# Performance work log

Measured on AMD Instinct MI355X. Metric: run time of the kernel, lower is better.

The kernel has to match this reference:

```python
import jax, jax.numpy as jnp
import numpy as np

# direction id -> (lat_shift, lon_shift)
WIND_DIRS = [(0, 0), (-1, 0), (-1, 1), (0, 1), (1, 1), (1, 0), (1, -1), (0, -1), (-1, -1)]
SWIN_SHIFT = (1, 3, 6)       # (pl, lat, lon)
WIND_SHIFT_SCALE = 2
LAT_REGIONS, LON_REGIONS = 4, 8
NUM_DIRS = 9


def setup_inputs() -> dict:
    key = jax.random.key(0)
    k1, k2 = jax.random.split(key)
    x = jax.random.normal(k1, (2, 14, 128, 256, 96), dtype=jnp.float32)
    wind_direction_id = jax.random.randint(k2, (2, 128, 256), 0, NUM_DIRS)
    return {"x": x, "wind_direction_id": wind_direction_id}


def _regional_dominant_dirs(wid):
    # wid: (B, H, W) int -> (B, LAT_REGIONS, LON_REGIONS) dominant direction per region
    B, H, W = wid.shape
    r = wid.reshape(B, LAT_REGIONS, H // LAT_REGIONS, LON_REGIONS, W // LON_REGIONS)
    counts = jnp.sum(jax.nn.one_hot(r, NUM_DIRS, dtype=jnp.float32), axis=(2, 4))  # (B, latR, lonR, 9)
    return jnp.argmax(counts, axis=-1)  # ties -> first max, matching torch bincount().argmax()


def reference(x, wind_direction_id):
    # x: (B, Pl, Lat, Lon, C); wind_direction_id: (B, H, W) in [0, 9)
    B, Pl, Lat, Lon, C = x.shape
    # 1) Swin fixed shift (negative roll on Pl, Lat, Lon)
    sp, sl, so = SWIN_SHIFT
    x = jnp.roll(x, (-sp, -sl, -so), axis=(1, 2, 3))
    # 2) per-region dominant wind direction
    rd = _regional_dominant_dirs(wind_direction_id)  # (B, latR, lonR)
    # nearest-neighbor upsample to full grid (matches F.interpolate mode='nearest')
    ih = (jnp.arange(Lat) * LAT_REGIONS) // Lat
    iw = (jnp.arange(Lon) * LON_REGIONS) // Lon
    dirs_up = rd[:, ih][:, :, iw]  # (B, Lat, Lon)
    # 3) mask & combine over the 9 rolled versions
    combined = jnp.zeros_like(x)
    for dir_id, (lat_s, lon_s) in enumerate(WIND_DIRS):
        als, alo = lat_s * WIND_SHIFT_SCALE, lon_s * WIND_SHIFT_SCALE
        shifted = x if (als == 0 and alo == 0) else jnp.roll(x, (als, alo), axis=(2, 3))
        mask = (dirs_up == dir_id).astype(x.dtype)[:, None, :, :, None]  # (B,1,Lat,Lon,1)
        combined = combined + shifted * mask
    # 4) global dominant direction (returned as stat)
    counts = jnp.bincount(wind_direction_id.reshape(-1), length=NUM_DIRS)
    dominant_id = jnp.argmax(counts)
    return combined, dominant_id
```

## Files before the change

kernel.cpp:

```cpp
#include <hip/hip_runtime.h>

namespace {
constexpr int kB   = 2;
constexpr int kPl  = 14;
constexpr int kLat = 128;
constexpr int kLon = 256;
constexpr int kC   = 96;
constexpr int kNumDirs = 9;
constexpr int kC4  = kC / 4;
constexpr int kNTotal = kB * kPl * kLat * kLon * kC;
constexpr int kRegions = kB * 4 * 8;
constexpr int kRowTasks = kB * kPl * kLat;
constexpr int kRowF4 = kLon * kC4;
constexpr int kRowIters = kRowF4 / 256;
}

typedef float f4 __attribute__((ext_vector_type(4)));

__device__ __constant__ int c_lat_s[kNumDirs] = {0,-1,-1, 0, 1, 1, 1, 0,-1};
__device__ __constant__ int c_lon_s[kNumDirs] = {0, 0, 1, 1, 1, 0,-1,-1,-1};

__global__ __launch_bounds__(256) void region_dirs_kernel(
        const int* __restrict__ wid, int* __restrict__ rdpack,
        int* __restrict__ cnt_blk) {
    __shared__ int cnt[kNumDirs];
    const int t = threadIdx.x;
    if (t < kNumDirs) cnt[t] = 0;
    __syncthreads();

    const int blk  = blockIdx.x;
    const int rlon = blk & 7;
    const int rlat = (blk >> 3) & 3;
    const int b    = blk >> 5;

    for (int k = t; k < 1024; k += 256) {
        const int i  = k >> 5;
        const int j  = k & 31;
        const int la = rlat * 32 + i;
        const int lo = rlon * 32 + j;
        atomicAdd(&cnt[wid[(b * kLat + la) * kLon + lo]], 1);
    }
    __syncthreads();

    if (t < kNumDirs) cnt_blk[blk * kNumDirs + t] = cnt[t];
    if (t == 0) {
        int best = 0, bestc = cnt[0];
        #pragma unroll
        for (int d = 1; d < kNumDirs; ++d)
            if (cnt[d] > bestc) { bestc = cnt[d]; best = d; }
        const int dla = 3 - 2 * c_lat_s[best];
        const int dlo = 6 - 2 * c_lon_s[best];
        rdpack[blk] = (dla << 8) | dlo;
    }
}

__global__ __launch_bounds__(256) void gather_rows_kernel(
        const f4* __restrict__ x, const int* __restrict__ rdpack,
        const int* __restrict__ cnt_blk, f4* __restrict__ out,
        float* __restrict__ out_dom) {
    if (blockIdx.x == kRowTasks) {
        __shared__ int tot[kNumDirs];
        const int t = threadIdx.x;
        if (t < kNumDirs) {
            int s = 0;
            for (int r = 0; r < kRegions; ++r) s += cnt_blk[r * kNumDirs + t];
            tot[t] = s;
        }
        __syncthreads();
        if (t == 0) {
            int best = 0, bestc = tot[0];
            #pragma unroll
            for (int d = 1; d < kNumDirs; ++d)
                if (tot[d] > bestc) { bestc = tot[d]; best = d; }
            *out_dom = (float)best;
        }
        return;
    }

    const int t   = threadIdx.x;
    const int blk = blockIdx.x;
    const int la  = blk & (kLat - 1);
    const int bp  = blk >> 7;
    const int p   = bp % kPl;
    const int b   = bp / kPl;
    int psrc = p + 1; if (psrc >= kPl) psrc = 0;

    __shared__ int s_pack8[8];
    if (t < 8) s_pack8[t] = rdpack[(b * 4 + (la >> 5)) * 8 + t];
    __syncthreads();

    const long srow = (long)((b * kPl + psrc) * kLat) * kRowF4;
    const long drow = (long)blk * kRowF4;

    #pragma unroll 6
    for (int k = 0; k < kRowIters; ++k) {
        const int flat = k * 256 + t;
        const int lo   = flat / kC4;
        const int c4   = flat - lo * kC4;

        const int pack  = s_pack8[lo >> 5];
        const int lasrc = (la + (pack >> 8)) & (kLat - 1);
        const int losrc = (lo + (pack & 0xff)) & (kLon - 1);

        const long src = srow + (long)lasrc * kRowF4 + losrc * kC4 + c4;
        const f4 v = x[src];
        __builtin_nontemporal_store(v, &out[drow + flat]);
    }
}

extern "C" void kernel_launch(void* const* d_in, const int* in_sizes, int n_in,
                              void* d_out, int out_size, void* d_ws, size_t ws_size,
                              hipStream_t stream) {
    const float* x   = (const float*)d_in[0];
    const int*   wid = (const int*)d_in[1];
    float* out = (float*)d_out;

    int* rdpack  = (int*)d_ws;
    int* cnt_blk = rdpack + kRegions;

    region_dirs_kernel<<<kRegions, 256, 0, stream>>>(wid, rdpack, cnt_blk);
    gather_rows_kernel<<<kRowTasks + 1, 256, 0, stream>>>(
        (const f4*)x, rdpack, cnt_blk, (f4*)out, out + kNTotal);
}
```

Before: 130.4 us.

## Fuse region-direction voting into gather kernel with per-block ballot histograms

Removes the separate region_dirs kernel and its workspace handoff. Each gather block now recomputes the dominant directions for its 8 lon-regions with wave-level ballot/popcount histograms, and the extra block computes the global histogram directly from wid. This drops one kernel launch and the inter-kernel dependency. In exchange, every row block redundantly reads 32K ints of wid (about 3584 blocks times 128KB, mostly from L2) before it starts its gather.

```diff
diff --git a/kernel.cpp b/kernel.cpp
--- a/kernel.cpp
+++ b/kernel.cpp
@@ -9,10 +9,10 @@
 constexpr int kNumDirs = 9;
 constexpr int kC4  = kC / 4;
 constexpr int kNTotal = kB * kPl * kLat * kLon * kC;
-constexpr int kRegions = kB * 4 * 8;
 constexpr int kRowTasks = kB * kPl * kLat;
 constexpr int kRowF4 = kLon * kC4;
 constexpr int kRowIters = kRowF4 / 256;
+constexpr int kWidTotal = kB * kLat * kLon;
 }
 
 typedef float f4 __attribute__((ext_vector_type(4)));
@@ -20,73 +20,85 @@
 __device__ __constant__ int c_lat_s[kNumDirs] = {0,-1,-1, 0, 1, 1, 1, 0,-1};
 __device__ __constant__ int c_lon_s[kNumDirs] = {0, 0, 1, 1, 1, 0,-1,-1,-1};
 
-__global__ __launch_bounds__(256) void region_dirs_kernel(
-        const int* __restrict__ wid, int* __restrict__ rdpack,
-        int* __restrict__ cnt_blk) {
-    __shared__ int cnt[kNumDirs];
-    const int t = threadIdx.x;
-    if (t < kNumDirs) cnt[t] = 0;
-    __syncthreads();
+__global__ __launch_bounds__(256) void fused_gather_kernel(
+        const f4* __restrict__ x, const int* __restrict__ wid,
+        f4* __restrict__ out, float* __restrict__ out_dom) {
+    const int t    = threadIdx.x;
+    const int wave = t >> 6;
+    const int lane = t & 63;
 
-    const int blk  = blockIdx.x;
-    const int rlon = blk & 7;
-    const int rlat = (blk >> 3) & 3;
-    const int b    = blk >> 5;
-
-    for (int k = t; k < 1024; k += 256) {
-        const int i  = k >> 5;
-        const int j  = k & 31;
-        const int la = rlat * 32 + i;
-        const int lo = rlon * 32 + j;
-        atomicAdd(&cnt[wid[(b * kLat + la) * kLon + lo]], 1);
-    }
-    __syncthreads();
-
-    if (t < kNumDirs) cnt_blk[blk * kNumDirs + t] = cnt[t];
-    if (t == 0) {
-        int best = 0, bestc = cnt[0];
+    if (blockIdx.x == kRowTasks) {
+        __shared__ int s_gcnt[4][kNumDirs];
+        int cnt[kNumDirs];
         #pragma unroll
-        for (int d = 1; d < kNumDirs; ++d)
-            if (cnt[d] > bestc) { bestc = cnt[d]; best = d; }
-        const int dla = 3 - 2 * c_lat_s[best];
-        const int dlo = 6 - 2 * c_lon_s[best];
-        rdpack[blk] = (dla << 8) | dlo;
-    }
-}
-
-__global__ __launch_bounds__(256) void gather_rows_kernel(
-        const f4* __restrict__ x, const int* __restrict__ rdpack,
-        const int* __restrict__ cnt_blk, f4* __restrict__ out,
-        float* __restrict__ out_dom) {
-    if (blockIdx.x == kRowTasks) {
-        __shared__ int tot[kNumDirs];
-        const int t = threadIdx.x;
-        if (t < kNumDirs) {
-            int s = 0;
-            for (int r = 0; r < kRegions; ++r) s += cnt_blk[r * kNumDirs + t];
-            tot[t] = s;
+        for (int d = 0; d < kNumDirs; ++d) cnt[d] = 0;
+        const int* w = wid + wave * (kWidTotal / 4);
+        for (int k = 0; k < kWidTotal / 4 / 64; ++k) {
+            const int v = w[k * 64 + lane];
+            #pragma unroll
+            for (int d = 0; d < kNumDirs; ++d)
+                cnt[d] += (int)__popcll(__ballot(v == d));
+        }
+        if (lane == 0) {
+            #pragma unroll
+            for (int d = 0; d < kNumDirs; ++d) s_gcnt[wave][d] = cnt[d];
         }
         __syncthreads();
         if (t == 0) {
-            int best = 0, bestc = tot[0];
+            int best = 0, bestc = -1;
             #pragma unroll
-            for (int d = 1; d < kNumDirs; ++d)
-                if (tot[d] > bestc) { bestc = tot[d]; best = d; }
+            for (int d = 0; d < kNumDirs; ++d) {
+                const int s = s_gcnt[0][d] + s_gcnt[1][d] + s_gcnt[2][d] + s_gcnt[3][d];
+                if (s > bestc) { bestc = s; best = d; }
+            }
             *out_dom = (float)best;
         }
         return;
     }
 
-    const int t   = threadIdx.x;
     const int blk = blockIdx.x;
     const int la  = blk & (kLat - 1);
     const int bp  = blk >> 7;
     const int p   = bp % kPl;
     const int b   = bp / kPl;
     int psrc = p + 1; if (psrc >= kPl) psrc = 0;
+    const int laR = la >> 5;
 
+    __shared__ int s_cnt[8][kNumDirs];
     __shared__ int s_pack8[8];
-    if (t < 8) s_pack8[t] = rdpack[(b * 4 + (la >> 5)) * 8 + t];
+    {
+        const int* wbase = wid + (b * kLat + laR * 32) * kLon;
+        #pragma unroll
+        for (int rr = 0; rr < 2; ++rr) {
+            const int r = wave * 2 + rr;
+            int cnt[kNumDirs];
+            #pragma unroll
+            for (int d = 0; d < kNumDirs; ++d) cnt[d] = 0;
+            const int* wreg = wbase + r * 32;
+            #pragma unroll
+            for (int k = 0; k < 16; ++k) {
+                const int idx = k * 64 + lane;
+                const int v = wreg[(idx >> 5) * kLon + (idx & 31)];
+                #pragma unroll
+                for (int d = 0; d < kNumDirs; ++d)
+                    cnt[d] += (int)__popcll(__ballot(v == d));
+            }
+            if (lane == 0) {
+                #pragma unroll
+                for (int d = 0; d < kNumDirs; ++d) s_cnt[r][d] = cnt[d];
+            }
+        }
+    }
+    __syncthreads();
+    if (t < 8) {
+        int best = 0, bestc = s_cnt[t][0];
+        #pragma unroll
+        for (int d = 1; d < kNumDirs; ++d)
+            if (s_cnt[t][d] > bestc) { bestc = s_cnt[t][d]; best = d; }
+        const int dla = 3 - 2 * c_lat_s[best];
+        const int dlo = 6 - 2 * c_lon_s[best];
+        s_pack8[t] = (dla << 8) | dlo;
+    }
     __syncthreads();
 
     const long srow = (long)((b * kPl + psrc) * kLat) * kRowF4;
@@ -115,10 +127,6 @@
     const int*   wid = (const int*)d_in[1];
     float* out = (float*)d_out;
 
-    int* rdpack  = (int*)d_ws;
-    int* cnt_blk = rdpack + kRegions;
-
-    region_dirs_kernel<<<kRegions, 256, 0, stream>>>(wid, rdpack, cnt_blk);
-    gather_rows_kernel<<<kRowTasks + 1, 256, 0, stream>>>(
-        (const f4*)x, rdpack, cnt_blk, (f4*)out, out + kNTotal);
+    fused_gather_kernel<<<kRowTasks + 1, 256, 0, stream>>>(
+        (const f4*)x, wid, (f4*)out, out + kNTotal);
 }
```

After: 159.2 us. +22.1%, slower.
